# Kernel optimization log

Measured on AMD Instinct MI355X. Metric: run time of the kernel, lower is better.

The kernel has to match this reference:

```python
import jax, jax.numpy as jnp
import numpy as np

OUT_DIM = 1024


def setup_inputs() -> dict:
    key = jax.random.key(0)
    k1, k2, k3, k4 = jax.random.split(key, 4)
    B, N, D = 4, 2048, 1024
    s = 1.0 / np.sqrt(D)
    return {
        "x": jax.random.normal(k1, (B, N, D), dtype=jnp.float32),
        "W_query": jax.random.normal(k2, (D, OUT_DIM), dtype=jnp.float32) * s,
        "W_key": jax.random.normal(k3, (D, OUT_DIM), dtype=jnp.float32) * s,
        "W_value": jax.random.normal(k4, (D, OUT_DIM), dtype=jnp.float32) * s,
    }


def reference(x, W_query, W_key, W_value):
    # x: [B, N, D_in]; W_*: [D_in, D_out] (torch Linear weight transposed)
    q = jnp.einsum("bnd,de->bne", x, W_query)
    k = jnp.einsum("bnd,de->bne", x, W_key)
    v = jnp.einsum("bnd,de->bne", x, W_value)
    sqrt_d = jnp.sqrt(jnp.asarray(OUT_DIM, dtype=jnp.float32))
    scores = jnp.einsum("bie,bje->bij", q, k) / sqrt_d  # [B, N, N]
    # NOTE: original uses softmax over dim=1 (query axis), not the usual dim=2
    attn = jax.nn.softmax(scores, axis=1)
    # dropout with train=False is identity (eval-mode reference)
    # out = attn^T @ v  ->  out[b, j] = sum_i attn[b, i, j] * v[b, i]
    return jnp.einsum("bij,bie->bje", attn, v)
```

## Files before the change

### kernel.cpp

```cpp
#include <hip/hip_runtime.h>
#include <math.h>


typedef __bf16 bf16x8 __attribute__((ext_vector_type(8)));
typedef float f32x4 __attribute__((ext_vector_type(4)));

static __device__ __forceinline__ unsigned short f2bf(float f) {
    unsigned u = __float_as_uint(f);
    u += 0x7fff + ((u >> 16) & 1);
    return (unsigned short)(u >> 16);
}

#define GLDS16(gptr, lptr)                                                            \
    __builtin_amdgcn_global_load_lds(                                                 \
        (const __attribute__((address_space(1))) void*)(gptr),                        \
        (__attribute__((address_space(3))) void*)(lptr), 16, 0, 0)

__device__ __forceinline__ void gemm256_core(
    const unsigned short* __restrict__ Ab,
    const unsigned short* __restrict__ Bb,
    const long ld, unsigned short* lds, f32x4 acc[8][4])
{
    const int tid  = threadIdx.x;
    const int w    = tid >> 6;
    const int lane = tid & 63;

    const int  rsub  = lane >> 2;
    const int  sgrp  = lane & 3;
    const int  colsw = ((sgrp ^ (rsub & 3)) * 8);
    const long rowoff = (long)(w * 16 + rsub);

    const unsigned short* apg = Ab + rowoff * ld + colsw;
    const unsigned short* bpg = Bb + rowoff * ld + colsw;

    unsigned short* dA = lds + w * 512;
    unsigned short* dB = lds + 16384 + w * 512;

    const int fr   = lane & 15;
    const int quad = lane >> 4;
    const int wm   = (w >> 2) * 128;
    const int wn   = (w & 3) * 64;
    const int aoff = (wm + fr) * 32 + ((quad ^ (fr & 3)) * 8);
    const int boff = (wn + fr) * 32 + ((quad ^ (fr & 3)) * 8);

#define STG_A(kt, kh, buf) do {                                             \
    const unsigned short* g_ = apg + (long)(kt) * 64 + (kh) * 32;           \
    unsigned short* d_ = dA + (buf) * 32768 + (kh) * 8192;                  \
    GLDS16(g_, d_); GLDS16(g_ + 128 * ld, d_ + 4096); } while (0)
#define STG_B(kt, kh, buf) do {                                             \
    const unsigned short* g_ = bpg + (long)(kt) * 64 + (kh) * 32;           \
    unsigned short* d_ = dB + (buf) * 32768 + (kh) * 8192;                  \
    GLDS16(g_, d_); GLDS16(g_ + 128 * ld, d_ + 4096); } while (0)

    bf16x8 af[4], bf[4];
#define LOADB(buf, ks) do {                                                 \
    const unsigned short* p_ = lds + 16384 + (buf) * 32768 + (ks) * 8192 + boff; \
    bf[0] = *(const bf16x8*)(p_);        bf[1] = *(const bf16x8*)(p_ + 512);     \
    bf[2] = *(const bf16x8*)(p_ + 1024); bf[3] = *(const bf16x8*)(p_ + 1536); } while (0)
#define LOADA(buf, ks, mh) do {                                             \
    const unsigned short* p_ = lds + (buf) * 32768 + (ks) * 8192 + (mh) * 2048 + aoff; \
    af[0] = *(const bf16x8*)(p_);        af[1] = *(const bf16x8*)(p_ + 512);     \
    af[2] = *(const bf16x8*)(p_ + 1024); af[3] = *(const bf16x8*)(p_ + 1536); } while (0)

#define MFMA16(mh) do {                                                     \
    __builtin_amdgcn_s_setprio(1);                                          \
    _Pragma("unroll") for (int m_ = 0; m_ < 4; m_++)                        \
    _Pragma("unroll") for (int n_ = 0; n_ < 4; n_++)                        \
        acc[(mh) * 4 + m_][n_] = __builtin_amdgcn_mfma_f32_16x16x32_bf16(   \
            af[m_], bf[n_], acc[(mh) * 4 + m_][n_], 0, 0, 0);               \
    __builtin_amdgcn_s_setprio(0); } while (0)

#define BARSYNC  __builtin_amdgcn_s_barrier()
#define WAITLGKM do { asm volatile("s_waitcnt lgkmcnt(0)" ::: "memory");    \
                      __builtin_amdgcn_sched_barrier(0); } while (0)
#define WAITV4   asm volatile("s_waitcnt vmcnt(4)" ::: "memory")

#pragma unroll
    for (int i = 0; i < 8; i++)
#pragma unroll
        for (int j = 0; j < 4; j++) acc[i][j] = f32x4{0.f, 0.f, 0.f, 0.f};

    STG_A(0, 0, 0); STG_B(0, 0, 0); STG_A(0, 1, 0); STG_B(0, 1, 0);
    STG_A(1, 0, 1); STG_B(1, 0, 1);
    asm volatile("s_waitcnt vmcnt(4)" ::: "memory");
    BARSYNC;

#pragma unroll 1
    for (int i = 0; i < 8; ++i) {
        const int t1 = 2 * i + 1;
        const int t2 = (2 * i + 2) & 15;
        const int t3 = (2 * i + 3) & 15;
        LOADB(0, 0); LOADA(0, 0, 0); STG_A(t1, 1, 1);
        BARSYNC; WAITLGKM; MFMA16(0); BARSYNC;
        LOADA(0, 0, 1); STG_B(t1, 1, 1);
        BARSYNC; WAITLGKM; MFMA16(1); BARSYNC;
        LOADB(0, 1); LOADA(0, 1, 0); STG_A(t2, 0, 0);
        BARSYNC; WAITLGKM; MFMA16(0); BARSYNC;
        LOADA(0, 1, 1); STG_B(t2, 0, 0);
        BARSYNC; WAITLGKM; MFMA16(1); WAITV4; BARSYNC;
        LOADB(1, 0); LOADA(1, 0, 0); STG_A(t2, 1, 0);
        BARSYNC; WAITLGKM; MFMA16(0); BARSYNC;
        LOADA(1, 0, 1); STG_B(t2, 1, 0);
        BARSYNC; WAITLGKM; MFMA16(1); BARSYNC;
        LOADB(1, 1); LOADA(1, 1, 0); STG_A(t3, 0, 1);
        BARSYNC; WAITLGKM; MFMA16(0); BARSYNC;
        LOADA(1, 1, 1); STG_B(t3, 0, 1);
        BARSYNC; WAITLGKM; MFMA16(1); WAITV4; BARSYNC;
    }
    asm volatile("s_waitcnt vmcnt(0)" ::: "memory");

#undef STG_A
#undef STG_B
#undef LOADB
#undef LOADA
#undef MFMA16
#undef BARSYNC
#undef WAITLGKM
#undef WAITV4
}

__global__ __launch_bounds__(512, 2) void gemm_qkv256(
    const unsigned short* __restrict__ A, const unsigned short* __restrict__ B,
    unsigned short* __restrict__ QK, unsigned short* __restrict__ Vt)
{
    __shared__ unsigned short lds[65536];
    const long gm0 = (long)blockIdx.y * 256;
    const long gn0 = (long)blockIdx.x * 256;

    f32x4 acc[8][4];
    gemm256_core(A + gm0 * 1024, B + gn0 * 1024, 1024, lds, acc);

    const int tid = threadIdx.x;
    const int w = tid >> 6, lane = tid & 63;
    const int fr = lane & 15, quad = lane >> 4;
    const int wm = (w >> 2) * 128, wn = (w & 3) * 64;

    if (gn0 < 2048) {
#pragma unroll
        for (int mi = 0; mi < 8; mi++) {
            const long rb = gm0 + wm + (mi >> 2) * 64 + (mi & 3) * 16 + quad * 4;
#pragma unroll
            for (int n = 0; n < 4; n++) {
                const long cb = gn0 + wn + n * 16 + fr;
#pragma unroll
                for (int rr = 0; rr < 4; rr++)
                    QK[(rb + rr) * 2048L + cb] = f2bf(acc[mi][n][rr]);
            }
        }
    } else {
#pragma unroll
        for (int mi = 0; mi < 8; mi++) {
            const long rb = gm0 + wm + (mi >> 2) * 64 + (mi & 3) * 16 + quad * 4;
#pragma unroll
            for (int n = 0; n < 4; n++) {
                const long ce = gn0 - 2048 + wn + n * 16 + fr;
                ushort4 o;
                o.x = f2bf(acc[mi][n][0]);
                o.y = f2bf(acc[mi][n][1]);
                o.z = f2bf(acc[mi][n][2]);
                o.w = f2bf(acc[mi][n][3]);
                *(ushort4*)&Vt[ce * 8192L + rb] = o;
            }
        }
    }
}

__global__ __launch_bounds__(512, 2) void gemm_scores256(
    const unsigned short* __restrict__ QKb, unsigned short* __restrict__ P,
    float* __restrict__ l)
{
    __shared__ unsigned short lds[65536];
    const int bz = blockIdx.z;
    const long gm0 = (long)blockIdx.y * 256;
    const long gn0 = (long)blockIdx.x * 256;

    const unsigned short* Ab = QKb + (long)bz * 2048 * 2048 + 1024 + gm0 * 2048;
    const unsigned short* Bb = QKb + (long)bz * 2048 * 2048 + gn0 * 2048;

    f32x4 acc[8][4];
    gemm256_core(Ab, Bb, 2048, lds, acc);

    const int tid = threadIdx.x;
    const int w = tid >> 6, lane = tid & 63;
    const int fr = lane & 15, quad = lane >> 4;
    const int wm = (w >> 2) * 128, wn = (w & 3) * 64;

    unsigned short* Pb = P + (long)bz * 2048 * 2048;
    float* lb = l + (long)bz * 2048;
    const float scale = 1.0f / 32.0f;
#pragma unroll
    for (int mi = 0; mi < 8; mi++) {
        const long rb = gm0 + wm + (mi >> 2) * 64 + (mi & 3) * 16 + quad * 4;
        float rs[4] = {0.f, 0.f, 0.f, 0.f};
#pragma unroll
        for (int n = 0; n < 4; n++) {
            const long cb = gn0 + wn + n * 16 + fr;
#pragma unroll
            for (int rr = 0; rr < 4; rr++) {
                float e = __expf(acc[mi][n][rr] * scale);
                rs[rr] += e;
                Pb[(rb + rr) * 2048L + cb] = f2bf(e);
            }
        }
#pragma unroll
        for (int rr = 0; rr < 4; rr++) {
#pragma unroll
            for (int m = 8; m > 0; m >>= 1) rs[rr] += __shfl_xor(rs[rr], m, 16);
        }
        if (fr == 0) {
#pragma unroll
            for (int rr = 0; rr < 4; rr++)
                atomicAdd(&lb[rb + rr], rs[rr]);
        }
    }
}

__global__ __launch_bounds__(256) void gemm_pv(
    const unsigned short* __restrict__ P, const unsigned short* __restrict__ Vt,
    const float* __restrict__ l, float* __restrict__ out)
{
    __shared__ unsigned short As[128 * 64];
    __shared__ unsigned short Bs[128 * 64];

    const int tid  = threadIdx.x;
    const int wave = tid >> 6;
    const int lane = tid & 63;
    const int bz   = blockIdx.z;
    const long gm0 = (long)blockIdx.y * 128;
    const long gn0 = (long)blockIdx.x * 128;

    const unsigned short* Ab = P + (long)bz * 2048 * 2048;
    const unsigned short* Bb = Vt + (long)bz * 2048;

    const int r = lane >> 3;
    const int s = lane & 7;
    const int cg = (s ^ r) * 8;
    const unsigned short* ap = Ab + (gm0 + wave * 32 + r) * 2048L + cg;
    const unsigned short* bp = Bb + (gn0 + wave * 32 + r) * 8192L + cg;
    unsigned short* asl = &As[wave * 2048];
    unsigned short* bsl = &Bs[wave * 2048];

    const int wm   = (wave & 1) * 64;
    const int wn   = (wave >> 1) * 64;
    const int fr   = lane & 15;
    const int quad = lane >> 4;
    const int sw   = fr & 7;

    f32x4 acc[4][4];
#pragma unroll
    for (int i = 0; i < 4; i++)
#pragma unroll
        for (int j = 0; j < 4; j++) acc[i][j] = f32x4{0.f, 0.f, 0.f, 0.f};

    for (int k0 = 0; k0 < 2048; k0 += 64) {
        GLDS16(ap, asl);
        GLDS16(ap + 8 * 2048L, asl + 512);
        GLDS16(ap + 16 * 2048L, asl + 1024);
        GLDS16(ap + 24 * 2048L, asl + 1536);
        GLDS16(bp, bsl);
        GLDS16(bp + 8 * 8192L, bsl + 512);
        GLDS16(bp + 16 * 8192L, bsl + 1024);
        GLDS16(bp + 24 * 8192L, bsl + 1536);
        ap += 64;
        bp += 64;
        __syncthreads();

#pragma unroll
        for (int t = 0; t < 2; t++) {
            const int qs = ((t * 4 + quad) ^ sw) * 8;
            bf16x8 af[4], bf[4];
#pragma unroll
            for (int i = 0; i < 4; i++)
                af[i] = *(const bf16x8*)&As[(wm + i * 16 + fr) * 64 + qs];
#pragma unroll
            for (int j = 0; j < 4; j++)
                bf[j] = *(const bf16x8*)&Bs[(wn + j * 16 + fr) * 64 + qs];
#pragma unroll
            for (int i = 0; i < 4; i++)
#pragma unroll
                for (int j = 0; j < 4; j++)
                    acc[i][j] = __builtin_amdgcn_mfma_f32_16x16x32_bf16(
                        af[i], bf[j], acc[i][j], 0, 0, 0);
        }
        __syncthreads();
    }

    float* Ob = out + (long)bz * 2048 * 1024;
    const float* lb = l + (long)bz * 2048;
    const long crow0 = gm0 + wm + quad * 4;
#pragma unroll
    for (int i = 0; i < 4; i++) {
        const long rb = crow0 + i * 16;
        float inv[4];
#pragma unroll
        for (int rr = 0; rr < 4; rr++) inv[rr] = 1.0f / lb[rb + rr];
#pragma unroll
        for (int j = 0; j < 4; j++) {
            const long cb = gn0 + wn + j * 16 + fr;
#pragma unroll
            for (int rr = 0; rr < 4; rr++)
                Ob[(rb + rr) * 1024L + cb] = acc[i][j][rr] * inv[rr];
        }
    }
}

__global__ __launch_bounds__(256) void prep(
    const float* __restrict__ x,
    const float* __restrict__ Wq, const float* __restrict__ Wk,
    const float* __restrict__ Wv,
    unsigned short* __restrict__ xb, unsigned short* __restrict__ Wqkvt,
    float* __restrict__ l)
{
    __shared__ float t[32][33];
    const int b = blockIdx.x;
    const int tid = threadIdx.x;
    if (b < 8192) {
        int i = b * 256 + tid;
        float4 v = ((const float4*)x)[i];
        ushort4 o;
        o.x = f2bf(v.x); o.y = f2bf(v.y); o.z = f2bf(v.z); o.w = f2bf(v.w);
        ((ushort4*)xb)[i] = o;
        return;
    }
    if (b == 8192 + 3072) {
        float4 z = {0.f, 0.f, 0.f, 0.f};
#pragma unroll
        for (int i = 0; i < 8; i++)
            ((float4*)l)[tid * 8 + i] = z;
        return;
    }
    int tix = b - 8192;
    const int w = tix >> 10;
    tix &= 1023;
    const float* W = (w == 0) ? Wq : (w == 1) ? Wk : Wv;
    unsigned short* Wt = Wqkvt + (long)w * 1024 * 1024;
    const int bx = (tix & 31) * 32;
    const int by = (tix >> 5) * 32;
    const int tx = tid & 31;
    const int ty = (tid >> 5) * 4;
#pragma unroll
    for (int j = 0; j < 4; j++)
        t[ty + j][tx] = W[(long)(by + ty + j) * 1024 + bx + tx];
    __syncthreads();
#pragma unroll
    for (int j = 0; j < 4; j++)
        Wt[(long)(bx + ty + j) * 1024 + by + tx] = f2bf(t[tx][ty + j]);
}

extern "C" void kernel_launch(void* const* d_in, const int* in_sizes, int n_in,
                              void* d_out, int out_size, void* d_ws,
                              size_t ws_size, hipStream_t stream)
{
    const float* x  = (const float*)d_in[0];
    const float* Wq = (const float*)d_in[1];
    const float* Wk = (const float*)d_in[2];
    const float* Wv = (const float*)d_in[3];
    float* out = (float*)d_out;

    const long M1 = 1024 * 1024;
    unsigned short* u     = (unsigned short*)d_ws;
    unsigned short* xb    = u;
    unsigned short* Wqkvt = u + 8 * M1;
    unsigned short* QKb   = Wqkvt + 3 * M1;
    unsigned short* Vtb   = QKb + 16 * M1;
    unsigned short* Pb    = Vtb + 8 * M1;
    float* l              = (float*)(Pb + 16 * M1);

    prep<<<dim3(8192 + 3072 + 1), dim3(256), 0, stream>>>(x, Wq, Wk, Wv, xb, Wqkvt, l);

    gemm_qkv256<<<dim3(12, 32), dim3(512), 0, stream>>>(xb, Wqkvt, QKb, Vtb);

    gemm_scores256<<<dim3(8, 8, 4), dim3(512), 0, stream>>>(QKb, Pb, l);

    gemm_pv<<<dim3(8, 16, 4), dim3(256), 0, stream>>>(Pb, Vtb, l, out);
}
```

Measured before the change: 250.1 us.

## Restructure 256x256 GEMM LDS layout to 64-wide k-tiles and add XCD-aware block mapping

The shared GEMM core now stages 256x64 k-tiles per buffer with an 8-way XOR swizzle and splits the MFMA work into mh/nh quadrants, each covering two k-substeps. This reduces LDS bank conflicts and changes how operands are reused between quadrant steps. The QKV and scores GEMMs now launch 1D grids and remap block IDs so blocks sharing operand rows land on the same XCD, aiming for better L2 locality. The new interleaved stage/load schedule is intricate, and a mistake in buffer or quadrant ordering could cause races or wrong results.

```diff
diff --git a/kernel.cpp b/kernel.cpp
--- a/kernel.cpp
+++ b/kernel.cpp
@@ -25,49 +25,50 @@
     const int w    = tid >> 6;
     const int lane = tid & 63;
 
-    const int  rsub  = lane >> 2;
-    const int  sgrp  = lane & 3;
-    const int  colsw = ((sgrp ^ (rsub & 3)) * 8);
-    const long rowoff = (long)(w * 16 + rsub);
-
-    const unsigned short* apg = Ab + rowoff * ld + colsw;
-    const unsigned short* bpg = Bb + rowoff * ld + colsw;
-
-    unsigned short* dA = lds + w * 512;
-    unsigned short* dB = lds + 16384 + w * 512;
-
-    const int fr   = lane & 15;
-    const int quad = lane >> 4;
-    const int wm   = (w >> 2) * 128;
-    const int wn   = (w & 3) * 64;
-    const int aoff = (wm + fr) * 32 + ((quad ^ (fr & 3)) * 8);
-    const int boff = (wn + fr) * 32 + ((quad ^ (fr & 3)) * 8);
-
-#define STG_A(kt, kh, buf) do {                                             \
-    const unsigned short* g_ = apg + (long)(kt) * 64 + (kh) * 32;           \
-    unsigned short* d_ = dA + (buf) * 32768 + (kh) * 8192;                  \
-    GLDS16(g_, d_); GLDS16(g_ + 128 * ld, d_ + 4096); } while (0)
-#define STG_B(kt, kh, buf) do {                                             \
-    const unsigned short* g_ = bpg + (long)(kt) * 64 + (kh) * 32;           \
-    unsigned short* d_ = dB + (buf) * 32768 + (kh) * 8192;                  \
-    GLDS16(g_, d_); GLDS16(g_ + 128 * ld, d_ + 4096); } while (0)
-
-    bf16x8 af[4], bf[4];
-#define LOADB(buf, ks) do {                                                 \
-    const unsigned short* p_ = lds + 16384 + (buf) * 32768 + (ks) * 8192 + boff; \
-    bf[0] = *(const bf16x8*)(p_);        bf[1] = *(const bf16x8*)(p_ + 512);     \
-    bf[2] = *(const bf16x8*)(p_ + 1024); bf[3] = *(const bf16x8*)(p_ + 1536); } while (0)
-#define LOADA(buf, ks, mh) do {                                             \
-    const unsigned short* p_ = lds + (buf) * 32768 + (ks) * 8192 + (mh) * 2048 + aoff; \
-    af[0] = *(const bf16x8*)(p_);        af[1] = *(const bf16x8*)(p_ + 512);     \
-    af[2] = *(const bf16x8*)(p_ + 1024); af[3] = *(const bf16x8*)(p_ + 1536); } while (0)
-
-#define MFMA16(mh) do {                                                     \
+    const int r  = lane >> 3;
+    const int s  = lane & 7;
+    const int cg = (s ^ r) * 8;
+
+    const int fr    = lane & 15;
+    const int quad  = lane >> 4;
+    const int sw    = fr & 7;
+    const int arow0 = (w >> 2) * 128;
+    const int brow0 = (w & 3) * 64;
+
+#define STG_A(t, mh, buf) do {                                              \
+    const int rb_ = (w >> 2) * 128 + (mh) * 64 + (w & 3) * 16;              \
+    const unsigned short* g_ = Ab + (long)(rb_ + r) * ld + (long)(t) * 64 + cg; \
+    unsigned short* d_ = lds + (buf) * 16384 + rb_ * 64;                    \
+    GLDS16(g_, d_); GLDS16(g_ + 8 * ld, d_ + 512); } while (0)
+#define STG_B(t, nh, buf) do {                                              \
+    const int rb_ = (w >> 1) * 64 + (nh) * 32 + (w & 1) * 16;               \
+    const unsigned short* g_ = Bb + (long)(rb_ + r) * ld + (long)(t) * 64 + cg; \
+    unsigned short* d_ = lds + 32768 + (buf) * 16384 + rb_ * 64;            \
+    GLDS16(g_, d_); GLDS16(g_ + 8 * ld, d_ + 512); } while (0)
+
+    bf16x8 af[4][2], bf[2][2];
+#define LOADA(buf, mh) do {                                                 \
+    _Pragma("unroll") for (int ks_ = 0; ks_ < 2; ks_++)                     \
+    _Pragma("unroll") for (int i_ = 0; i_ < 4; i_++)                        \
+        af[i_][ks_] = *(const bf16x8*)&lds[(buf) * 16384 +                  \
+            (arow0 + (mh) * 64 + i_ * 16 + fr) * 64 +                       \
+            ((ks_ * 4 + quad) ^ sw) * 8]; } while (0)
+#define LOADB(buf, nh) do {                                                 \
+    _Pragma("unroll") for (int ks_ = 0; ks_ < 2; ks_++)                     \
+    _Pragma("unroll") for (int j_ = 0; j_ < 2; j_++)                        \
+        bf[j_][ks_] = *(const bf16x8*)&lds[32768 + (buf) * 16384 +          \
+            (brow0 + (nh) * 32 + j_ * 16 + fr) * 64 +                       \
+            ((ks_ * 4 + quad) ^ sw) * 8]; } while (0)
+
+#define MFMA16(mh, nh) do {                                                 \
     __builtin_amdgcn_s_setprio(1);                                          \
-    _Pragma("unroll") for (int m_ = 0; m_ < 4; m_++)                        \
-    _Pragma("unroll") for (int n_ = 0; n_ < 4; n_++)                        \
-        acc[(mh) * 4 + m_][n_] = __builtin_amdgcn_mfma_f32_16x16x32_bf16(   \
-            af[m_], bf[n_], acc[(mh) * 4 + m_][n_], 0, 0, 0);               \
+    _Pragma("unroll") for (int ks_ = 0; ks_ < 2; ks_++)                     \
+    _Pragma("unroll") for (int i_ = 0; i_ < 4; i_++)                        \
+    _Pragma("unroll") for (int j_ = 0; j_ < 2; j_++)                        \
+        acc[(mh) * 4 + i_][(nh) * 2 + j_] =                                 \
+            __builtin_amdgcn_mfma_f32_16x16x32_bf16(                        \
+                af[i_][ks_], bf[j_][ks_],                                   \
+                acc[(mh) * 4 + i_][(nh) * 2 + j_], 0, 0, 0);                \
     __builtin_amdgcn_s_setprio(0); } while (0)
 
 #define BARSYNC  __builtin_amdgcn_s_barrier()
@@ -80,8 +81,8 @@
 #pragma unroll
         for (int j = 0; j < 4; j++) acc[i][j] = f32x4{0.f, 0.f, 0.f, 0.f};
 
-    STG_A(0, 0, 0); STG_B(0, 0, 0); STG_A(0, 1, 0); STG_B(0, 1, 0);
-    STG_A(1, 0, 1); STG_B(1, 0, 1);
+    STG_A(0, 0, 0); STG_A(0, 1, 0); STG_B(0, 0, 0); STG_B(0, 1, 0);
+    STG_A(1, 0, 1); STG_B(1, 1, 1);
     asm volatile("s_waitcnt vmcnt(4)" ::: "memory");
     BARSYNC;
 
@@ -90,29 +91,29 @@
         const int t1 = 2 * i + 1;
         const int t2 = (2 * i + 2) & 15;
         const int t3 = (2 * i + 3) & 15;
-        LOADB(0, 0); LOADA(0, 0, 0); STG_A(t1, 1, 1);
-        BARSYNC; WAITLGKM; MFMA16(0); BARSYNC;
-        LOADA(0, 0, 1); STG_B(t1, 1, 1);
-        BARSYNC; WAITLGKM; MFMA16(1); BARSYNC;
-        LOADB(0, 1); LOADA(0, 1, 0); STG_A(t2, 0, 0);
-        BARSYNC; WAITLGKM; MFMA16(0); BARSYNC;
-        LOADA(0, 1, 1); STG_B(t2, 0, 0);
-        BARSYNC; WAITLGKM; MFMA16(1); WAITV4; BARSYNC;
-        LOADB(1, 0); LOADA(1, 0, 0); STG_A(t2, 1, 0);
-        BARSYNC; WAITLGKM; MFMA16(0); BARSYNC;
-        LOADA(1, 0, 1); STG_B(t2, 1, 0);
-        BARSYNC; WAITLGKM; MFMA16(1); BARSYNC;
-        LOADB(1, 1); LOADA(1, 1, 0); STG_A(t3, 0, 1);
-        BARSYNC; WAITLGKM; MFMA16(0); BARSYNC;
-        LOADA(1, 1, 1); STG_B(t3, 0, 1);
-        BARSYNC; WAITLGKM; MFMA16(1); WAITV4; BARSYNC;
+        LOADA(0, 0); LOADB(0, 0); STG_B(t1, 0, 1);
+        BARSYNC; WAITLGKM; MFMA16(0, 0); BARSYNC;
+        LOADB(0, 1); STG_A(t1, 1, 1);
+        BARSYNC; WAITLGKM; MFMA16(0, 1); BARSYNC;
+        LOADA(0, 1); STG_A(t2, 0, 0);
+        BARSYNC; WAITLGKM; MFMA16(1, 1); BARSYNC;
+        LOADB(0, 0); STG_B(t2, 1, 0);
+        BARSYNC; WAITLGKM; MFMA16(1, 0); WAITV4; BARSYNC;
+        LOADA(1, 0); LOADB(1, 0); STG_A(t2, 1, 0);
+        BARSYNC; WAITLGKM; MFMA16(0, 0); BARSYNC;
+        LOADB(1, 1); STG_B(t2, 0, 0);
+        BARSYNC; WAITLGKM; MFMA16(0, 1); BARSYNC;
+        LOADA(1, 1); STG_A(t3, 0, 1);
+        BARSYNC; WAITLGKM; MFMA16(1, 1); BARSYNC;
+        LOADB(1, 0); STG_B(t3, 1, 1);
+        BARSYNC; WAITLGKM; MFMA16(1, 0); WAITV4; BARSYNC;
     }
     asm volatile("s_waitcnt vmcnt(0)" ::: "memory");
 
 #undef STG_A
 #undef STG_B
+#undef LOADA
 #undef LOADB
-#undef LOADA
 #undef MFMA16
 #undef BARSYNC
 #undef WAITLGKM
@@ -124,8 +125,11 @@
     unsigned short* __restrict__ QK, unsigned short* __restrict__ Vt)
 {
     __shared__ unsigned short lds[65536];
-    const long gm0 = (long)blockIdx.y * 256;
-    const long gn0 = (long)blockIdx.x * 256;
+    const int orig = blockIdx.x;
+    const int xcd  = orig & 7;
+    const int pos  = orig >> 3;
+    const long gm0 = (long)(xcd * 4 + (pos & 3)) * 256;
+    const long gn0 = (long)(pos >> 2) * 256;
 
     f32x4 acc[8][4];
     gemm256_core(A + gm0 * 1024, B + gn0 * 1024, 1024, lds, acc);
@@ -170,9 +174,12 @@
     float* __restrict__ l)
 {
     __shared__ unsigned short lds[65536];
-    const int bz = blockIdx.z;
-    const long gm0 = (long)blockIdx.y * 256;
-    const long gn0 = (long)blockIdx.x * 256;
+    const int orig = blockIdx.x;
+    const int xcd  = orig & 7;
+    const int pos  = orig >> 3;
+    const int bz   = xcd >> 1;
+    const long gm0 = (long)((xcd & 1) * 4 + (pos >> 3)) * 256;
+    const long gn0 = (long)(pos & 7) * 256;
 
     const unsigned short* Ab = QKb + (long)bz * 2048 * 2048 + 1024 + gm0 * 2048;
     const unsigned short* Bb = QKb + (long)bz * 2048 * 2048 + gn0 * 2048;
@@ -368,9 +375,9 @@
 
     prep<<<dim3(8192 + 3072 + 1), dim3(256), 0, stream>>>(x, Wq, Wk, Wv, xb, Wqkvt, l);
 
-    gemm_qkv256<<<dim3(12, 32), dim3(512), 0, stream>>>(xb, Wqkvt, QKb, Vtb);
-
-    gemm_scores256<<<dim3(8, 8, 4), dim3(512), 0, stream>>>(QKb, Pb, l);
+    gemm_qkv256<<<dim3(384), dim3(512), 0, stream>>>(xb, Wqkvt, QKb, Vtb);
+
+    gemm_scores256<<<dim3(256), dim3(512), 0, stream>>>(QKb, Pb, l);
 
     gemm_pv<<<dim3(8, 16, 4), dim3(256), 0, stream>>>(Pb, Vtb, l, out);
 }
```

After: 236.5 us. 5.4% less time.
